# Performance work log

Hardware: AMD Instinct MI355X
Metric: run time of the kernel (lower is better)

## Reference

```python
import jax, jax.numpy as jnp
import numpy as np

NUM_GRAPHS = 1024
EPS = 1e-5  # BatchNorm eps
NEG_SLOPE = 0.2  # GATConv leaky_relu slope


def _bn(x, g, b):
    # train-mode BatchNorm over node/graph axis (biased variance, as torch)
    mu = jnp.mean(x, axis=0)
    var = jnp.mean((x - mu) ** 2, axis=0)
    return (x - mu) * jax.lax.rsqrt(var + EPS) * g + b


def _prelu(x, a):
    return jnp.where(x > 0, x, a * x)


def _gat_layer(x, src, dst, W, a_src, a_dst, bias, n_nodes):
    # single-head GATConv (heads=1, concat=True), self-loops already in src/dst
    h = x @ W                                            # [N, C]
    e = jax.nn.leaky_relu(jnp.take(h @ a_src, src) + jnp.take(h @ a_dst, dst), NEG_SLOPE)  # [E]
    m = jax.ops.segment_max(e, dst, num_segments=n_nodes)
    ex = jnp.exp(e - jnp.take(m, dst))
    denom = jax.ops.segment_sum(ex, dst, num_segments=n_nodes)
    alpha = ex / (jnp.take(denom, dst) + 1e-16)          # softmax over in-edges of each target
    out = jax.ops.segment_sum(jnp.take(h, src, axis=0) * alpha[:, None], dst, num_segments=n_nodes)
    return out + bias


def setup_inputs() -> dict:
    key = jax.random.key(0)
    ks = jax.random.split(key, 16)
    N, E, F, H, C = 500_000, 8_000_000, 7, 8, 2

    def gl(k, shp, fan_in):
        return (jax.random.normal(k, shp, jnp.float32) / np.sqrt(fan_in)).astype(jnp.float32)

    return {
        "x": jax.random.normal(ks[0], (N, F), jnp.float32),
        "edge_index": jax.random.randint(ks[1], (2, E), 0, N, jnp.int32),
        "batch": jnp.sort(jax.random.randint(ks[2], (N,), 0, NUM_GRAPHS, jnp.int32)),
        "W1": gl(ks[3], (F, H), F), "as1": gl(ks[4], (H,), H), "ad1": gl(ks[5], (H,), H), "b1": jnp.zeros((H,), jnp.float32),
        "W2": gl(ks[6], (H, H), H), "as2": gl(ks[7], (H,), H), "ad2": gl(ks[8], (H,), H), "b2": jnp.zeros((H,), jnp.float32),
        "W3": gl(ks[9], (H, H), H), "as3": gl(ks[10], (H,), H), "ad3": gl(ks[11], (H,), H), "b3": jnp.zeros((H,), jnp.float32),
        "g1": jnp.ones((H,), jnp.float32), "be1": jnp.zeros((H,), jnp.float32),
        "g2": jnp.ones((H,), jnp.float32), "be2": jnp.zeros((H,), jnp.float32),
        "g3": jnp.ones((H,), jnp.float32), "be3": jnp.zeros((H,), jnp.float32),
        "a_gnn": jnp.float32(0.25),
        "Wjk": gl(ks[12], (3 * H, H), 3 * H), "bjk": jnp.zeros((H,), jnp.float32),
        "Wm1": gl(ks[13], (H, H), H), "bm1": jnp.zeros((H,), jnp.float32),
        "gm": jnp.ones((H,), jnp.float32), "bem": jnp.zeros((H,), jnp.float32),
        "a_mlp": jnp.float32(0.25),
        "Wm2": gl(ks[14], (H, C), H), "bm2": jnp.zeros((C,), jnp.float32),
    }


def reference(x, edge_index, batch,
              W1, as1, ad1, b1, W2, as2, ad2, b2, W3, as3, ad3, b3,
              g1, be1, g2, be2, g3, be3, a_gnn, Wjk, bjk,
              Wm1, bm1, gm, bem, a_mlp, Wm2, bm2):
    N = x.shape[0]
    loop = jnp.arange(N, dtype=edge_index.dtype)  # GATConv add_self_loops=True
    src = jnp.concatenate([edge_index[0], loop])
    dst = jnp.concatenate([edge_index[1], loop])
    # 3-layer GAT, each: conv -> BatchNorm -> PReLU (dropout omitted: eval)
    h1 = _prelu(_bn(_gat_layer(x, src, dst, W1, as1, ad1, b1, N), g1, be1), a_gnn)
    h2 = _prelu(_bn(_gat_layer(h1, src, dst, W2, as2, ad2, b2, N), g2, be2), a_gnn)
    h3 = _prelu(_bn(_gat_layer(h2, src, dst, W3, as3, ad3, b3, N), g3, be3), a_gnn)
    # JumpingKnowledge 'cat' + projection to out_channels
    h = jnp.concatenate([h1, h2, h3], axis=1) @ Wjk + bjk   # [N, 8]
    pooled = jax.ops.segment_sum(h, batch, num_segments=NUM_GRAPHS)  # global_add_pool [G, 8]
    m1 = _prelu(_bn(pooled @ Wm1 + bm1, gm, bem), a_mlp)    # MLP hidden
    return m1 @ Wm2 + bm2                                    # [G, 2] logits
```

## Files before the change

### kernel.cpp

```cpp
#include <hip/hip_runtime.h>

typedef unsigned short u16;
typedef unsigned int   u32;

#define EPSBN     1e-5f
#define NEG_SLOPE 0.2f
#define NGRAPH    1024
#define NPB       512
#define CHUNK     16384
#define BKCAP     11264
#define NTILE     8
#define SLOTS     1536


static __device__ __forceinline__ float bfl(const u16* __restrict__ p, int i){
    return __uint_as_float(((u32)p[i]) << 16);
}
static __device__ __forceinline__ float ldf(const void* __restrict__ p, int i, bool f32){
    return f32 ? ((const float*)p)[i] : bfl((const u16*)p, i);
}
static __device__ __forceinline__ u16 f2bf(float f){
    u32 u = __float_as_uint(f);
    return (u16)((u + 0x7fffu + ((u >> 16) & 1u)) >> 16);
}
static __device__ __forceinline__ void unpack8(uint4 pk, float* a){
    a[0] = __uint_as_float((pk.x & 0xffffu) << 16);
    a[1] = __uint_as_float( pk.x & 0xffff0000u);
    a[2] = __uint_as_float((pk.y & 0xffffu) << 16);
    a[3] = __uint_as_float( pk.y & 0xffff0000u);
    a[4] = __uint_as_float((pk.z & 0xffffu) << 16);
    a[5] = __uint_as_float( pk.z & 0xffff0000u);
    a[6] = __uint_as_float((pk.w & 0xffffu) << 16);
    a[7] = __uint_as_float( pk.w & 0xffff0000u);
}
static __device__ __forceinline__ uint4 pack8(const float* a){
    uint4 pk;
    pk.x = (u32)f2bf(a[0]) | ((u32)f2bf(a[1])<<16);
    pk.y = (u32)f2bf(a[2]) | ((u32)f2bf(a[3])<<16);
    pk.z = (u32)f2bf(a[4]) | ((u32)f2bf(a[5])<<16);
    pk.w = (u32)f2bf(a[6]) | ((u32)f2bf(a[7])<<16);
    return pk;
}

static __device__ __forceinline__ int wave_scan_incl(int x){
    int lane = threadIdx.x & 63;
    #pragma unroll
    for (int off = 1; off < 64; off <<= 1){
        int y = __shfl_up(x, off, 64);
        if (lane >= off) x += y;
    }
    return x;
}
static __device__ __forceinline__ int block_scan_incl(int x, int* wpart){
    int t = threadIdx.x, lane = t & 63, wv = t >> 6;
    int nw = blockDim.x >> 6;
    int ws = wave_scan_incl(x);
    __syncthreads();
    if (lane == 63) wpart[wv] = ws;
    __syncthreads();
    if (wv == 0){
        int p = (lane < nw) ? wpart[lane] : 0;
        p = wave_scan_incl(p);
        if (lane < nw) wpart[lane] = p;
    }
    __syncthreads();
    int base = wv ? wpart[wv-1] : 0;
    return base + ws;
}

__global__ void k_sniff(const u16* __restrict__ x, int* __restrict__ flag){
    int lane = threadIdx.x;
    bool hit = false;
    for (int i = lane; i < 128; i += 64){
        float v = bfl(x, i);
        if (!(fabsf(v) <= 1e6f)) hit = true;
    }
    unsigned long long m = __ballot(hit);
    if (lane == 0) flag[0] = (m != 0ull) ? 1 : 0;
}

__global__ __launch_bounds__(1024) void k_binsort(const int* __restrict__ src,
                                                  const int* __restrict__ dst,
                                                  u32* __restrict__ stage,
                                                  int* __restrict__ matL,
                                                  int E, int B){
    __shared__ u32 pr[CHUNK];
    __shared__ int h[2048];
    __shared__ int wpart[16];
    int c = blockIdx.x, t = threadIdx.x;
    int e0 = c << 14, e1 = min(e0 + CHUNK, E), cn = e1 - e0;
    for (int b = t; b < B; b += 1024) h[b] = 0;
    __syncthreads();
    for (int i = e0 + t; i < e1; i += 1024) atomicAdd(&h[dst[i] >> 9], 1);
    __syncthreads();
    int base = t << 1, run = 0, loc[2];
    #pragma unroll
    for (int j = 0; j < 2; j++){
        int b = base + j;
        int v = (b < B) ? h[b] : 0;
        loc[j] = run; run += v;
    }
    int incl = block_scan_incl(run, wpart);
    int bex = incl - run;
    __syncthreads();
    #pragma unroll
    for (int j = 0; j < 2; j++){
        int b = base + j;
        if (b < B) h[b] = bex + loc[j];
    }
    __syncthreads();
    int* mrow = matL + (size_t)c * (B+1);
    for (int b = t; b < B; b += 1024) mrow[b] = h[b];
    if (t == 0) mrow[B] = cn;
    __syncthreads();
    for (int i = e0 + t; i < e1; i += 1024){
        int d = dst[i];
        int b = d >> 9;
        int p = atomicAdd(&h[b], 1);
        pr[p] = ((u32)src[i] << 9) | (u32)(d & 511);
    }
    __syncthreads();
    u32* srow = stage + ((size_t)c << 14);
    for (int i = t; i < cn; i += 1024) srow[i] = pr[i];
}

__global__ __launch_bounds__(256) void k_mtrans(const int* __restrict__ matL,
                                                int* __restrict__ matT, int R, int C){
    __shared__ int tile[32][33];
    int tx = threadIdx.x & 31, ty = threadIdx.x >> 5;
    int c0 = blockIdx.x << 5, r0 = blockIdx.y << 5;
    for (int j = ty; j < 32; j += 8){
        int r = r0 + j, c = c0 + tx;
        if (r < C && c < R) tile[j][tx] = matL[(size_t)r*R + c];
    }
    __syncthreads();
    for (int j = ty; j < 32; j += 8){
        int cc = c0 + j, rr = r0 + tx;
        if (cc < R && rr < C) matT[(size_t)cc*C + rr] = tile[tx][j];
    }
}

__global__ __launch_bounds__(256) void k_bucketsum(const int* __restrict__ matT,
                                                   int* __restrict__ bb, int B, int NC){
    int b = blockIdx.x, t = threadIdx.x;
    __shared__ int s[256];
    int acc = 0;
    const int* r0 = matT + (size_t)b*NC;
    const int* r1 = matT + (size_t)(b+1)*NC;
    for (int c = t; c < NC; c += 256) acc += r1[c] - r0[c];
    s[t] = acc; __syncthreads();
    for (int off = 128; off > 0; off >>= 1){
        if (t < off) s[t] += s[t+off];
        __syncthreads();
    }
    if (t == 0) bb[b] = s[0];
}

__global__ __launch_bounds__(1024) void k_bktbase(int* __restrict__ bb, int B,
                                                  float* __restrict__ statsAll){
    __shared__ int wpart[16];
    int t = threadIdx.x;
    if (t < 48) statsAll[t] = 0.f;
    int v = (t < B) ? bb[t] : 0;
    int incl = block_scan_incl(v, wpart);
    if (t < B) bb[t] = incl - v;
    if (t == B-1) bb[B] = incl;
}

__global__ __launch_bounds__(1024) void k_bucket(const u32* __restrict__ stage,
                                                 const int* __restrict__ matT,
                                                 const int* __restrict__ bb,
                                                 int* __restrict__ tileOfs,
                                                 u32* __restrict__ csr,
                                                 int N, int B, int NC){
    __shared__ u32 pr[BKCAP];
    __shared__ int hist[4096];
    __shared__ int sc[1024];
    __shared__ int lofsA[512];
    __shared__ int wpart[16];
    int k = blockIdx.x, t = threadIdx.x;
    int n0 = k << 9, n1 = min(n0 + NPB, N), nn = n1 - n0;
    int cnt = 0, lofs = 0;
    if (t < NC){
        lofs = matT[(size_t)k*NC + t];
        cnt  = matT[(size_t)(k+1)*NC + t] - lofs;
    }
    if (t < 512) lofsA[t] = lofs;
    int incl1 = block_scan_incl(cnt, wpart);
    sc[t] = incl1;
    __syncthreads();
    int total = sc[1023];
    int ec    = min(total, BKCAP - nn);
    for (int pidx = t; pidx < ec; pidx += 1024){
        int lo = 0, hi = 511;
        while (lo < hi){ int mid = (lo + hi) >> 1; if (sc[mid] > pidx) hi = mid; else lo = mid + 1; }
        int segStart = lo ? sc[lo-1] : 0;
        pr[pidx] = stage[((size_t)lo << 14) + lofsA[lo] + (pidx - segStart)];
    }
    __syncthreads();
    for (int j = t; j < nn; j += 1024) pr[ec + j] = ((u32)(n0 + j) << 9) | (u32)j;
    int ecnt = ec + nn;
    for (int i = t; i < 4096; i += 1024) hist[i] = 0;
    __syncthreads();
    for (int i = t; i < ecnt; i += 1024){
        u32 pk = pr[i];
        int dl = pk & 511;
        int tile = min((int)(pk >> 9) >> 16, NTILE-1);
        atomicAdd(&hist[(tile << 9) + dl], 1);
    }
    __syncthreads();
    int base = t << 2, run = 0, loc[4];
    #pragma unroll
    for (int j = 0; j < 4; j++){ loc[j] = run; run += hist[base + j]; }
    int incl2 = block_scan_incl(run, wpart);
    int bex = incl2 - run;
    __syncthreads();
    #pragma unroll
    for (int j = 0; j < 4; j++) hist[base + j] = bex + loc[j];
    if ((t & 127) == 0) tileOfs[(size_t)k*9 + (t >> 7)] = bex;
    if (t == 0)         tileOfs[(size_t)k*9 + 8] = ecnt;
    __syncthreads();
    int wbase = bb[k] + n0;
    for (int i = t; i < ecnt; i += 1024){
        u32 pk = pr[i];
        int dl = pk & 511;
        int tile = min((int)(pk >> 9) >> 16, NTILE-1);
        int p = atomicAdd(&hist[(tile << 9) + dl], 1);
        csr[wbase + p] = pk;
    }
}

__global__ void k_transform(const uint4* __restrict__ actpk, const void* __restrict__ xraw,
                            const int* __restrict__ dflag, int fin,
                            const void* __restrict__ W, const void* __restrict__ adst,
                            const float* __restrict__ stats, const void* __restrict__ gamma,
                            const void* __restrict__ beta, const void* __restrict__ alpha,
                            uint4* __restrict__ hrec, float* __restrict__ hd, int n){
    const bool f32 = dflag[0] != 0;
    __shared__ float Wl[64], dl[8], scl[8], sft[8], alv;
    int t = threadIdx.x;
    if (t < 64)            Wl[t]   = (t < fin*8) ? ldf(W, t, f32) : 0.f;
    if (t >= 64 && t < 72) dl[t-64] = ldf(adst, t-64, f32);
    if (t == 80) alv = ldf(alpha, 0, f32);
    if (stats && t < 8){
        float invN = 1.f/(float)n;
        float mu  = stats[t]*invN;
        float var = fmaxf(stats[8+t]*invN - mu*mu, 0.f);
        float s   = ldf(gamma, t, f32)*rsqrtf(var + EPSBN);
        scl[t] = s; sft[t] = ldf(beta, t, f32) - mu*s;
    }
    __syncthreads();
    int i = blockIdx.x*blockDim.x + t;
    if (i >= n) return;
    float a[8];
    if (xraw){
        #pragma unroll
        for (int k=0;k<7;k++) a[k] = ldf(xraw, i*7 + k, f32);
        a[7] = 0.f;
    } else {
        unpack8(actpk[i], a);
        #pragma unroll
        for (int j=0;j<8;j++){
            float y = a[j]*scl[j] + sft[j];
            a[j] = (y > 0.f) ? y : alv*y;
        }
    }
    float h[8];
    #pragma unroll
    for (int j=0;j<8;j++){
        float acc = 0.f;
        #pragma unroll
        for (int k=0;k<8;k++) acc += a[k]*Wl[k*8+j];
        h[j] = acc;
    }
    float s2 = 0.f;
    #pragma unroll
    for (int j=0;j<8;j++) s2 += h[j]*dl[j];
    hd[i] = s2;
    hrec[i] = pack8(h);
}

__global__ __launch_bounds__(512) void k_aggregate(
        const u32* __restrict__ csr, const int* __restrict__ bb,
        const int* __restrict__ tileOfs,
        const uint4* __restrict__ hrec, const float* __restrict__ hd,
        const void* __restrict__ asrc, const int* __restrict__ dflag,
        uint4* __restrict__ act, float* __restrict__ stats, int n){
    const bool f32 = dflag[0] != 0;
    __shared__ u32   stg[4*SLOTS];
    __shared__ float swp[SLOTS];
    __shared__ u16   sdl[SLOTS];
    __shared__ float hdl[512];
    __shared__ u16 bs[512], be[512];
    __shared__ float alS[8];
    __shared__ float sred[8][16];
    __shared__ int tofS[9];
    int k = blockIdx.x, t = threadIdx.x;
    int n0 = k << 9;
    int nn = min(NPB, n - n0);
    if (t < 8) alS[t] = ldf(asrc, t, f32);
    if (t < 9) tofS[t] = tileOfs[(size_t)k*9 + t];
    hdl[t] = (t < nn) ? hd[n0 + t] : 0.f;
    int e0 = bb[k] + n0;
    __syncthreads();
    float al[8];
    #pragma unroll
    for (int j = 0; j < 8; j++) al[j] = alS[j];
    float acc[8] = {0,0,0,0,0,0,0,0};
    float den = 0.f;

    int wt = 0, wc = 0;
    while (wt < NTILE && wc >= tofS[wt+1]){ wt++; if (wt < NTILE) wc = tofS[wt]; }

    u32 pkc[3]; uint4 hvc[3];
    if (wt < NTILE){
        int L = min(SLOTS, tofS[wt+1] - wc);
        #pragma unroll
        for (int j = 0; j < 3; j++) pkc[j] = csr[e0 + wc + min(t + (j << 9), L - 1)];
        #pragma unroll
        for (int j = 0; j < 3; j++) hvc[j] = hrec[pkc[j] >> 9];
    }

    while (wt < NTILE){
        int L = min(SLOTS, tofS[wt+1] - wc);
        __syncthreads();
        #pragma unroll
        for (int j = 0; j < 3; j++){
            int i = t + (j << 9);
            float h[8]; unpack8(hvc[j], h);
            int dl = (int)(pkc[j] & 511u);
            float e = hdl[dl];
            #pragma unroll
            for (int q = 0; q < 8; q++) e += h[q]*al[q];
            e = (e > 0.f) ? e : NEG_SLOPE*e;
            float w = __expf(e);
            if (i < L){
                stg[0*SLOTS + i] = hvc[j].x;
                stg[1*SLOTS + i] = hvc[j].y;
                stg[2*SLOTS + i] = hvc[j].z;
                stg[3*SLOTS + i] = hvc[j].w;
                swp[i] = w;
                sdl[i] = (u16)dl;
            }
        }
        bs[t] = 0; be[t] = 0;
        __syncthreads();
        int nwt = wt, nwc = wc + SLOTS;
        while (nwt < NTILE && nwc >= tofS[nwt+1]){ nwt++; if (nwt < NTILE) nwc = tofS[nwt]; }
        if (nwt < NTILE){
            int Ln = min(SLOTS, tofS[nwt+1] - nwc);
            #pragma unroll
            for (int j = 0; j < 3; j++) pkc[j] = csr[e0 + nwc + min(t + (j << 9), Ln - 1)];
            #pragma unroll
            for (int j = 0; j < 3; j++) hvc[j] = hrec[pkc[j] >> 9];
        }
        for (int i = t; i < L; i += 512){
            int dl = (int)sdl[i];
            if (i == 0){
                bs[dl] = 0;
            } else {
                int dp = (int)sdl[i - 1];
                if (dp != dl){ bs[dl] = (u16)i; be[dp] = (u16)i; }
            }
            if (i == L-1) be[dl] = (u16)L;
        }
        __syncthreads();
        {
            int p0 = bs[t], p1 = be[t];
            for (int p = p0; p < p1; ++p){
                uint4 hv = make_uint4(stg[0*SLOTS + p], stg[1*SLOTS + p],
                                      stg[2*SLOTS + p], stg[3*SLOTS + p]);
                float h[8]; unpack8(hv, h);
                float w = swp[p];
                den += w;
                #pragma unroll
                for (int q = 0; q < 8; q++) acc[q] += w*h[q];
            }
        }
        wt = nwt; wc = nwc;
    }

    float o[8] = {0,0,0,0,0,0,0,0};
    if (t < nn){
        float inv = 1.f/(den + 1e-16f);
        #pragma unroll
        for (int j = 0; j < 8; j++) o[j] = acc[j]*inv;
        act[n0 + t] = pack8(o);
    }
    float v[16];
    #pragma unroll
    for (int j=0;j<8;j++){ v[j]=o[j]; v[8+j]=o[j]*o[j]; }
    #pragma unroll
    for (int off=32; off>0; off>>=1){
        #pragma unroll
        for (int j=0;j<16;j++) v[j] += __shfl_down(v[j], off, 64);
    }
    int lane = t & 63, wv = t >> 6;
    if (lane == 0){
        #pragma unroll
        for (int j=0;j<16;j++) sred[wv][j] = v[j];
    }
    __syncthreads();
    if (t < 16){
        float tot = 0.f;
        #pragma unroll
        for (int w=0; w<8; w++) tot += sred[w][t];
        atomicAdd(&stats[t], tot);
    }
}

static __device__ __forceinline__ int lowerb(const int* __restrict__ a, int n, int key){
    int lo = 0, hi = n;
    while (lo < hi){ int mid = (lo + hi) >> 1; if (a[mid] < key) lo = mid + 1; else hi = mid; }
    return lo;
}

__global__ __launch_bounds__(256) void k_jkpool(
        const uint4* __restrict__ a1, const uint4* __restrict__ a2, const uint4* __restrict__ a3,
        const float* __restrict__ st1, const float* __restrict__ st2, const float* __restrict__ st3,
        const void* __restrict__ g1, const void* __restrict__ be1,
        const void* __restrict__ g2, const void* __restrict__ be2,
        const void* __restrict__ g3, const void* __restrict__ be3,
        const void* __restrict__ alpha,
        const void* __restrict__ Wjk, const void* __restrict__ bjk,
        const int* __restrict__ dflag,
        const int* __restrict__ batch, float* __restrict__ pooled, int n){
    const bool f32 = dflag[0] != 0;
    __shared__ float Wl[192], bl[8], scl[24], sft[24], alv;
    __shared__ int rng[2];
    int t = threadIdx.x, g = blockIdx.x;
    if (t < 192) Wl[t] = ldf(Wjk, t, f32);
    if (t < 8)   bl[t] = ldf(bjk, t, f32);
    if (t < 24){
        int L = t >> 3, j = t & 7;
        const float* st = (L==0)? st1 : (L==1)? st2 : st3;
        const void* gg  = (L==0)? g1  : (L==1)? g2  : g3;
        const void* bb_ = (L==0)? be1 : (L==1)? be2 : be3;
        float invN = 1.f/(float)n;
        float mu  = st[j]*invN;
        float var = fmaxf(st[8+j]*invN - mu*mu, 0.f);
        float s   = ldf(gg, j, f32)*rsqrtf(var + EPSBN);
        scl[t] = s; sft[t] = ldf(bb_, j, f32) - mu*s;
    }
    if (t == 30) alv = ldf(alpha, 0, f32);
    if (t == 0) rng[0] = lowerb(batch, n, g);
    if (t == 1) rng[1] = lowerb(batch, n, g+1);
    __syncthreads();
    int lo = rng[0], hi = rng[1];
    float pa[8] = {0,0,0,0,0,0,0,0};
    for (int i = lo + t; i < hi; i += 256){
        float c[24];
        unpack8(a1[i], c);
        unpack8(a2[i], c+8);
        unpack8(a3[i], c+16);
        #pragma unroll
        for (int k=0;k<24;k++){
            float y = c[k]*scl[k] + sft[k];
            c[k] = (y > 0.f) ? y : alv*y;
        }
        #pragma unroll
        for (int j=0;j<8;j++){
            float acc = bl[j];
            #pragma unroll
            for (int k=0;k<24;k++) acc += c[k]*Wl[k*8+j];
            pa[j] += acc;
        }
    }
    #pragma unroll
    for (int off=32; off>0; off>>=1){
        #pragma unroll
        for (int j=0;j<8;j++) pa[j] += __shfl_down(pa[j], off, 64);
    }
    __shared__ float sr[4][8];
    int lane = t & 63, wv = t >> 6;
    if (lane == 0){
        #pragma unroll
        for (int j=0;j<8;j++) sr[wv][j] = pa[j];
    }
    __syncthreads();
    if (t < 8){
        float tot = sr[0][t]+sr[1][t]+sr[2][t]+sr[3][t];
        pooled[(size_t)g*8 + t] = tot;
    }
}

__global__ __launch_bounds__(1024) void k_final(
        const float* __restrict__ pooled,
        const void* __restrict__ Wm1, const void* __restrict__ bm1,
        const void* __restrict__ gm, const void* __restrict__ bem,
        const void* __restrict__ am,
        const void* __restrict__ Wm2, const void* __restrict__ bm2,
        const int* __restrict__ dflag,
        float* __restrict__ out, int G){
    const bool f32 = dflag[0] != 0;
    int t = threadIdx.x;
    float tv[8] = {0,0,0,0,0,0,0,0};
    if (t < G){
        float r[8];
        #pragma unroll
        for (int j=0;j<8;j++) r[j] = pooled[(size_t)t*8+j];
        #pragma unroll
        for (int j=0;j<8;j++){
            float acc = ldf(bm1, j, f32);
            #pragma unroll
            for (int k=0;k<8;k++) acc += r[k]*ldf(Wm1, k*8+j, f32);
            tv[j] = acc;
        }
    }
    float v[16];
    #pragma unroll
    for (int j=0;j<8;j++){ v[j]=tv[j]; v[8+j]=tv[j]*tv[j]; }
    #pragma unroll
    for (int off=32; off>0; off>>=1){
        #pragma unroll
        for (int j=0;j<16;j++) v[j] += __shfl_down(v[j], off, 64);
    }
    __shared__ float sred[16][16];
    int lane = t & 63, wv = t >> 6;
    if (lane == 0){
        #pragma unroll
        for (int j=0;j<16;j++) sred[wv][j] = v[j];
    }
    __syncthreads();
    __shared__ float stt[16];
    if (t < 16){
        float tot = 0.f;
        #pragma unroll
        for (int w=0; w<16; w++) tot += sred[w][t];
        stt[t] = tot;
    }
    __syncthreads();
    if (t < G){
        float a = ldf(am, 0, f32);
        float invG = 1.f/(float)G;
        float m1[8];
        #pragma unroll
        for (int j=0;j<8;j++){
            float mu  = stt[j]*invG;
            float var = fmaxf(stt[8+j]*invG - mu*mu, 0.f);
            float y = (tv[j]-mu)*rsqrtf(var+EPSBN)*ldf(gm,j,f32)+ldf(bem,j,f32);
            m1[j] = (y>0.f)? y : a*y;
        }
        #pragma unroll
        for (int c=0;c<2;c++){
            float oacc = ldf(bm2, c, f32);
            #pragma unroll
            for (int k=0;k<8;k++) oacc += m1[k]*ldf(Wm2, k*2+c, f32);
            out[(size_t)t*2+c] = oacc;
        }
    }
}

extern "C" void kernel_launch(void* const* d_in, const int* in_sizes, int n_in,
                              void* d_out, int out_size, void* d_ws, size_t ws_size,
                              hipStream_t stream){
    const u16* x16   = (const u16*)d_in[0];
    const void* x    = d_in[0];
    const int* ei    = (const int*)d_in[1];
    const int* batch = (const int*)d_in[2];
    int N = in_sizes[2];
    int E = in_sizes[1] / 2;
    const int* srcA = ei;
    const int* dstA = ei + E;
    const void *W1=d_in[3],  *as1=d_in[4],  *ad1=d_in[5];
    const void *W2=d_in[7],  *as2=d_in[8],  *ad2=d_in[9];
    const void *W3=d_in[11], *as3=d_in[12], *ad3=d_in[13];
    const void *g1=d_in[15], *be1=d_in[16];
    const void *g2=d_in[17], *be2=d_in[18];
    const void *g3=d_in[19], *be3=d_in[20];
    const void *agnn=d_in[21];
    const void *Wjk=d_in[22], *bjk=d_in[23];
    const void *Wm1=d_in[24], *bm1=d_in[25];
    const void *gm =d_in[26], *bem=d_in[27];
    const void *amlp=d_in[28];
    const void *Wm2=d_in[29], *bm2=d_in[30];

    char* p = (char*)d_ws;
    auto carve = [&](size_t bytes) -> void* {
        void* r = (void*)p;
        p += (bytes + 255) & ~(size_t)255;
        return r;
    };
    size_t M = (size_t)E + (size_t)N;
    int nb512 = (N + 511)/512;
    int B  = (N + NPB - 1) / NPB;
    int NC = (E + CHUNK - 1) / CHUNK;
    int*   dflag  = (int*)  carve(256);
    int*   bb     = (int*)  carve(((size_t)B+1)*4);
    int*   tileOfs= (int*)  carve((size_t)B*9*4);
    int*   matL   = (int*)  carve((size_t)NC*(B+1)*4);
    int*   matT   = (int*)  carve((size_t)(B+1)*NC*4);
    u32*   stage  = (u32*)  carve((size_t)NC*CHUNK*4);
    u32*   csr    = (u32*)  carve(M*4);
    uint4* hrec   = (uint4*)carve((size_t)N*16);
    float* hd     = (float*)carve((size_t)N*4);
    uint4* act1   = (uint4*)carve((size_t)N*16);
    uint4* act2   = (uint4*)carve((size_t)N*16);
    uint4* act3   = (uint4*)carve((size_t)N*16);
    float* statsA = (float*)carve(256);
    float* stats1 = statsA;
    float* stats2 = statsA + 16;
    float* stats3 = statsA + 32;
    float* pooled = (float*)carve((size_t)NGRAPH*32);
    (void)ws_size; (void)n_in;

    k_sniff<<<1, 64, 0, stream>>>(x16, dflag);

    k_binsort  <<<NC, 1024, 0, stream>>>(srcA, dstA, stage, matL, E, B);
    {
        dim3 tg(((B+1) + 31)/32, (NC + 31)/32);
        k_mtrans<<<tg, 256, 0, stream>>>(matL, matT, B+1, NC);
    }
    k_bucketsum<<<B, 256, 0, stream>>>(matT, bb, B, NC);
    k_bktbase  <<<1, 1024, 0, stream>>>(bb, B, statsA);
    k_bucket   <<<B, 1024, 0, stream>>>(stage, matT, bb, tileOfs, csr, N, B, NC);

    k_transform <<<nb512, 512, 0, stream>>>(nullptr, x, dflag, 7, W1, ad1,
                                            nullptr, nullptr, nullptr, agnn, hrec, hd, N);
    k_aggregate <<<B, 512, 0, stream>>>(csr, bb, tileOfs, hrec, hd, as1, dflag, act1, stats1, N);
    k_transform <<<nb512, 512, 0, stream>>>(act1, nullptr, dflag, 8, W2, ad2,
                                            stats1, g1, be1, agnn, hrec, hd, N);
    k_aggregate <<<B, 512, 0, stream>>>(csr, bb, tileOfs, hrec, hd, as2, dflag, act2, stats2, N);
    k_transform <<<nb512, 512, 0, stream>>>(act2, nullptr, dflag, 8, W3, ad3,
                                            stats2, g2, be2, agnn, hrec, hd, N);
    k_aggregate <<<B, 512, 0, stream>>>(csr, bb, tileOfs, hrec, hd, as3, dflag, act3, stats3, N);

    k_jkpool<<<NGRAPH, 256, 0, stream>>>(act1, act2, act3, stats1, stats2, stats3,
                                         g1, be1, g2, be2, g3, be3, agnn,
                                         Wjk, bjk, dflag, batch, pooled, N);
    int G = out_size / 2;
    k_final <<<1, 1024, 0, stream>>>(pooled, Wm1, bm1, gm, bem, amlp, Wm2, bm2, dflag, (float*)d_out, G);
}
```

Baseline: 523.5 us.

## Drop transpose/prefix kernels by using fixed-capacity per-bucket CSR slots

Removes the matrix transpose, bucket-sum and bucket-base scan kernels by giving each destination bucket a fixed BKCAP-sized slot in the CSR buffer. k_bucket now reads per-chunk offsets directly (strided) from the untransposed matL. The dtype sniff and stats zeroing are folded into block 0 of k_binsort. This cuts four kernel launches and their global round trips, at the cost of a larger padded CSR allocation and strided matL reads.

```diff
diff --git a/kernel.cpp b/kernel.cpp
--- a/kernel.cpp
+++ b/kernel.cpp
@@ -68,26 +68,30 @@
     return base + ws;
 }
 
-__global__ void k_sniff(const u16* __restrict__ x, int* __restrict__ flag){
-    int lane = threadIdx.x;
-    bool hit = false;
-    for (int i = lane; i < 128; i += 64){
-        float v = bfl(x, i);
-        if (!(fabsf(v) <= 1e6f)) hit = true;
-    }
-    unsigned long long m = __ballot(hit);
-    if (lane == 0) flag[0] = (m != 0ull) ? 1 : 0;
-}
-
 __global__ __launch_bounds__(1024) void k_binsort(const int* __restrict__ src,
                                                   const int* __restrict__ dst,
                                                   u32* __restrict__ stage,
                                                   int* __restrict__ matL,
-                                                  int E, int B){
+                                                  int E, int B,
+                                                  const u16* __restrict__ x16,
+                                                  int* __restrict__ dflag,
+                                                  float* __restrict__ statsAll){
     __shared__ u32 pr[CHUNK];
     __shared__ int h[2048];
     __shared__ int wpart[16];
     int c = blockIdx.x, t = threadIdx.x;
+    if (c == 0){
+        if (t < 64){
+            bool hit = false;
+            for (int i = t; i < 128; i += 64){
+                float v = bfl(x16, i);
+                if (!(fabsf(v) <= 1e6f)) hit = true;
+            }
+            unsigned long long m = __ballot(hit);
+            if (t == 0) dflag[0] = (m != 0ull) ? 1 : 0;
+        }
+        if (t >= 64 && t < 112) statsAll[t - 64] = 0.f;
+    }
     int e0 = c << 14, e1 = min(e0 + CHUNK, E), cn = e1 - e0;
     for (int b = t; b < B; b += 1024) h[b] = 0;
     __syncthreads();
@@ -124,52 +128,8 @@
     for (int i = t; i < cn; i += 1024) srow[i] = pr[i];
 }
 
-__global__ __launch_bounds__(256) void k_mtrans(const int* __restrict__ matL,
-                                                int* __restrict__ matT, int R, int C){
-    __shared__ int tile[32][33];
-    int tx = threadIdx.x & 31, ty = threadIdx.x >> 5;
-    int c0 = blockIdx.x << 5, r0 = blockIdx.y << 5;
-    for (int j = ty; j < 32; j += 8){
-        int r = r0 + j, c = c0 + tx;
-        if (r < C && c < R) tile[j][tx] = matL[(size_t)r*R + c];
-    }
-    __syncthreads();
-    for (int j = ty; j < 32; j += 8){
-        int cc = c0 + j, rr = r0 + tx;
-        if (cc < R && rr < C) matT[(size_t)cc*C + rr] = tile[tx][j];
-    }
-}
-
-__global__ __launch_bounds__(256) void k_bucketsum(const int* __restrict__ matT,
-                                                   int* __restrict__ bb, int B, int NC){
-    int b = blockIdx.x, t = threadIdx.x;
-    __shared__ int s[256];
-    int acc = 0;
-    const int* r0 = matT + (size_t)b*NC;
-    const int* r1 = matT + (size_t)(b+1)*NC;
-    for (int c = t; c < NC; c += 256) acc += r1[c] - r0[c];
-    s[t] = acc; __syncthreads();
-    for (int off = 128; off > 0; off >>= 1){
-        if (t < off) s[t] += s[t+off];
-        __syncthreads();
-    }
-    if (t == 0) bb[b] = s[0];
-}
-
-__global__ __launch_bounds__(1024) void k_bktbase(int* __restrict__ bb, int B,
-                                                  float* __restrict__ statsAll){
-    __shared__ int wpart[16];
-    int t = threadIdx.x;
-    if (t < 48) statsAll[t] = 0.f;
-    int v = (t < B) ? bb[t] : 0;
-    int incl = block_scan_incl(v, wpart);
-    if (t < B) bb[t] = incl - v;
-    if (t == B-1) bb[B] = incl;
-}
-
 __global__ __launch_bounds__(1024) void k_bucket(const u32* __restrict__ stage,
-                                                 const int* __restrict__ matT,
-                                                 const int* __restrict__ bb,
+                                                 const int* __restrict__ matL,
                                                  int* __restrict__ tileOfs,
                                                  u32* __restrict__ csr,
                                                  int N, int B, int NC){
@@ -182,8 +142,8 @@
     int n0 = k << 9, n1 = min(n0 + NPB, N), nn = n1 - n0;
     int cnt = 0, lofs = 0;
     if (t < NC){
-        lofs = matT[(size_t)k*NC + t];
-        cnt  = matT[(size_t)(k+1)*NC + t] - lofs;
+        lofs = matL[(size_t)t*(B+1) + k];
+        cnt  = matL[(size_t)t*(B+1) + k + 1] - lofs;
     }
     if (t < 512) lofsA[t] = lofs;
     int incl1 = block_scan_incl(cnt, wpart);
@@ -220,7 +180,7 @@
     if ((t & 127) == 0) tileOfs[(size_t)k*9 + (t >> 7)] = bex;
     if (t == 0)         tileOfs[(size_t)k*9 + 8] = ecnt;
     __syncthreads();
-    int wbase = bb[k] + n0;
+    size_t wbase = (size_t)k * BKCAP;
     for (int i = t; i < ecnt; i += 1024){
         u32 pk = pr[i];
         int dl = pk & 511;
@@ -281,7 +241,7 @@
 }
 
 __global__ __launch_bounds__(512) void k_aggregate(
-        const u32* __restrict__ csr, const int* __restrict__ bb,
+        const u32* __restrict__ csr,
         const int* __restrict__ tileOfs,
         const uint4* __restrict__ hrec, const float* __restrict__ hd,
         const void* __restrict__ asrc, const int* __restrict__ dflag,
@@ -301,7 +261,7 @@
     if (t < 8) alS[t] = ldf(asrc, t, f32);
     if (t < 9) tofS[t] = tileOfs[(size_t)k*9 + t];
     hdl[t] = (t < nn) ? hd[n0 + t] : 0.f;
-    int e0 = bb[k] + n0;
+    const u32* ecsr = csr + (size_t)k * BKCAP;
     __syncthreads();
     float al[8];
     #pragma unroll
@@ -316,7 +276,7 @@
     if (wt < NTILE){
         int L = min(SLOTS, tofS[wt+1] - wc);
         #pragma unroll
-        for (int j = 0; j < 3; j++) pkc[j] = csr[e0 + wc + min(t + (j << 9), L - 1)];
+        for (int j = 0; j < 3; j++) pkc[j] = ecsr[wc + min(t + (j << 9), L - 1)];
         #pragma unroll
         for (int j = 0; j < 3; j++) hvc[j] = hrec[pkc[j] >> 9];
     }
@@ -350,7 +310,7 @@
         if (nwt < NTILE){
             int Ln = min(SLOTS, tofS[nwt+1] - nwc);
             #pragma unroll
-            for (int j = 0; j < 3; j++) pkc[j] = csr[e0 + nwc + min(t + (j << 9), Ln - 1)];
+            for (int j = 0; j < 3; j++) pkc[j] = ecsr[nwc + min(t + (j << 9), Ln - 1)];
             #pragma unroll
             for (int j = 0; j < 3; j++) hvc[j] = hrec[pkc[j] >> 9];
         }
@@ -581,17 +541,14 @@
         p += (bytes + 255) & ~(size_t)255;
         return r;
     };
-    size_t M = (size_t)E + (size_t)N;
     int nb512 = (N + 511)/512;
     int B  = (N + NPB - 1) / NPB;
     int NC = (E + CHUNK - 1) / CHUNK;
     int*   dflag  = (int*)  carve(256);
-    int*   bb     = (int*)  carve(((size_t)B+1)*4);
     int*   tileOfs= (int*)  carve((size_t)B*9*4);
     int*   matL   = (int*)  carve((size_t)NC*(B+1)*4);
-    int*   matT   = (int*)  carve((size_t)(B+1)*NC*4);
     u32*   stage  = (u32*)  carve((size_t)NC*CHUNK*4);
-    u32*   csr    = (u32*)  carve(M*4);
+    u32*   csr    = (u32*)  carve((size_t)B*BKCAP*4);
     uint4* hrec   = (uint4*)carve((size_t)N*16);
     float* hd     = (float*)carve((size_t)N*4);
     uint4* act1   = (uint4*)carve((size_t)N*16);
@@ -604,26 +561,18 @@
     float* pooled = (float*)carve((size_t)NGRAPH*32);
     (void)ws_size; (void)n_in;
 
-    k_sniff<<<1, 64, 0, stream>>>(x16, dflag);
-
-    k_binsort  <<<NC, 1024, 0, stream>>>(srcA, dstA, stage, matL, E, B);
-    {
-        dim3 tg(((B+1) + 31)/32, (NC + 31)/32);
-        k_mtrans<<<tg, 256, 0, stream>>>(matL, matT, B+1, NC);
-    }
-    k_bucketsum<<<B, 256, 0, stream>>>(matT, bb, B, NC);
-    k_bktbase  <<<1, 1024, 0, stream>>>(bb, B, statsA);
-    k_bucket   <<<B, 1024, 0, stream>>>(stage, matT, bb, tileOfs, csr, N, B, NC);
+    k_binsort <<<NC, 1024, 0, stream>>>(srcA, dstA, stage, matL, E, B, x16, dflag, statsA);
+    k_bucket  <<<B, 1024, 0, stream>>>(stage, matL, tileOfs, csr, N, B, NC);
 
     k_transform <<<nb512, 512, 0, stream>>>(nullptr, x, dflag, 7, W1, ad1,
                                             nullptr, nullptr, nullptr, agnn, hrec, hd, N);
-    k_aggregate <<<B, 512, 0, stream>>>(csr, bb, tileOfs, hrec, hd, as1, dflag, act1, stats1, N);
+    k_aggregate <<<B, 512, 0, stream>>>(csr, tileOfs, hrec, hd, as1, dflag, act1, stats1, N);
     k_transform <<<nb512, 512, 0, stream>>>(act1, nullptr, dflag, 8, W2, ad2,
                                             stats1, g1, be1, agnn, hrec, hd, N);
-    k_aggregate <<<B, 512, 0, stream>>>(csr, bb, tileOfs, hrec, hd, as2, dflag, act2, stats2, N);
+    k_aggregate <<<B, 512, 0, stream>>>(csr, tileOfs, hrec, hd, as2, dflag, act2, stats2, N);
     k_transform <<<nb512, 512, 0, stream>>>(act2, nullptr, dflag, 8, W3, ad3,
                                             stats2, g2, be2, agnn, hrec, hd, N);
-    k_aggregate <<<B, 512, 0, stream>>>(csr, bb, tileOfs, hrec, hd, as3, dflag, act3, stats3, N);
+    k_aggregate <<<B, 512, 0, stream>>>(csr, tileOfs, hrec, hd, as3, dflag, act3, stats3, N);
 
     k_jkpool<<<NGRAPH, 256, 0, stream>>>(act1, act2, act3, stats1, stats2, stats3,
                                          g1, be1, g2, be2, g3, be3, agnn,
```

Measured after the change: 514.0 us. Within noise of the previous version (-1.8%).
